# Kernel optimization log

Hardware: AMD Instinct MI355X
Metric: run time of the kernel (lower is better)

Reference implementation:

```python
import jax, jax.numpy as jnp
import numpy as np
from jax import lax

WINDOW_SIZE = 11
SIGMA = 1.5
C1 = 0.01 ** 2
C2 = 0.03 ** 2


def _gaussian_window(channel, window_size, sigma=SIGMA):
    x = jnp.arange(window_size, dtype=jnp.float32)
    g = jnp.exp(-((x - window_size // 2) ** 2) / (2.0 * sigma * sigma))
    g = g / g.sum()
    w2d = jnp.outer(g, g)  # [ws, ws]
    # depthwise kernel in OIHW with feature_group_count=channel: [C, 1, ws, ws]
    return jnp.broadcast_to(w2d[None, None], (channel, 1, window_size, window_size))


def _dwconv(x, window, pad, channel):
    return lax.conv_general_dilated(
        x, window, window_strides=(1, 1), padding=[(pad, pad), (pad, pad)],
        dimension_numbers=("NCHW", "OIHW", "NCHW"), feature_group_count=channel)


def setup_inputs() -> dict:
    key = jax.random.key(0)
    k1, k2 = jax.random.split(key)
    shape = (16, 3, 512, 512)
    img1 = jax.random.uniform(k1, shape, dtype=jnp.float32)
    img2 = jax.random.uniform(k2, shape, dtype=jnp.float32)
    return {"img1": img1, "img2": img2}


def reference(img1, img2):
    _, channel, height, width = img1.shape
    ws = min(WINDOW_SIZE, height, width)
    window = _gaussian_window(channel, ws).astype(img1.dtype)
    pad = WINDOW_SIZE // 2  # matches torch code: padding=window_size // 2

    mu1 = _dwconv(img1, window, pad, channel)
    mu2 = _dwconv(img2, window, pad, channel)
    mu1_sq = mu1 * mu1
    mu2_sq = mu2 * mu2
    mu1_mu2 = mu1 * mu2

    sigma1_sq = _dwconv(img1 * img1, window, pad, channel) - mu1_sq
    sigma2_sq = _dwconv(img2 * img2, window, pad, channel) - mu2_sq
    sigma12 = _dwconv(img1 * img2, window, pad, channel) - mu1_mu2

    ssim_map = ((2.0 * mu1_mu2 + C1) * (2.0 * sigma12 + C2)) / (
        (mu1_sq + mu2_sq + C1) * (sigma1_sq + sigma2_sq + C2))
    return 1.0 - ssim_map.mean()
```

## Files before the change

kernel.cpp:

```cpp
#include <hip/hip_runtime.h>
#include <hip/hip_fp16.h>


#define IMGH 512
#define IMGW 512
#define TW 64
#define TH 32
#define GX 8
#define GY 16
#define GZ 48
#define NBLOCKS (GX * GY * GZ)
#define NPIX (16 * 3 * 512 * 512)
#define C1F 1.0e-4f
#define C2F 9.0e-4f

#define INSTRIDE 88
#define INPLANE (42 * INSTRIDE)
#define VSTRIDE 44
#define VPLANE (64 * VSTRIDE)
#define WBASE 34

#define W0 0.0010283818f
#define W1 0.0075987503f
#define W2 0.0360007547f
#define W3 0.1093606960f
#define W4 0.2130055367f
#define W5 0.2660117184f

typedef _Float16 half8v __attribute__((ext_vector_type(8)));
typedef float f32x4 __attribute__((ext_vector_type(4)));
union H8 { half8v v; __half2 h2[4]; float4 f4; unsigned u[4]; };

static __device__ __forceinline__ __half2 pkrtz(float a, float b) {
    auto r = __builtin_amdgcn_cvt_pkrtz(a, b);
    return *reinterpret_cast<__half2*>(&r);
}
static __device__ __forceinline__ float wval(int i) {
    const float W[11] = {W0, W1, W2, W3, W4, W5, W4, W3, W2, W1, W0};
    float w = 0.f;
#pragma unroll
    for (int j = 0; j < 11; ++j) w = (i == WBASE + j) ? W[j] : w;
    return w;
}

__global__ __launch_bounds__(512, 8)
void ssim_tile(const float* __restrict__ img1, const float* __restrict__ img2,
               float* __restrict__ partials) {
    __shared__ _Float16 sWext[96];
    __shared__ _Float16 sIn[2 * INPLANE];
    __shared__ _Float16 sV[4 * VPLANE];
    __shared__ float wsum[8];

    const int tid  = threadIdx.x;
    const int lane = tid & 63;
    const int wv   = tid >> 6;
    const int lr = lane & 15;
    const int kc = lane >> 4;
    const int r0 = blockIdx.y * TH;
    const int c0 = blockIdx.x * TW;
    const size_t pbase = (size_t)blockIdx.z * (IMGH * IMGW);
    const float* a0 = img1 + pbase;
    const float* b0 = img2 + pbase;
    const bool fast = (blockIdx.x >= 1) & (blockIdx.x <= GX - 2) &
                      (blockIdx.y >= 1) & (blockIdx.y <= GY - 2);

    if (tid < 420) {
        const int row = (unsigned)tid / 10u;
        const int ch  = tid - row * 10;
        const int gr = r0 - 5 + row;
        const int gc = c0 - 8 + 8 * ch;
        f32x4 va1, va2, vb1, vb2;
        if (fast) {
            const float* pa = a0 + (size_t)gr * IMGW + gc;
            const float* pb = b0 + (size_t)gr * IMGW + gc;
            asm volatile(
                "global_load_dwordx4 %0, %4, off\n\t"
                "global_load_dwordx4 %1, %4, off offset:16\n\t"
                "global_load_dwordx4 %2, %5, off\n\t"
                "global_load_dwordx4 %3, %5, off offset:16\n\t"
                "s_waitcnt vmcnt(0)"
                : "=&v"(va1), "=&v"(va2), "=&v"(vb1), "=&v"(vb2)
                : "v"(pa), "v"(pb)
                : "memory");
        } else {
            va1 = (f32x4){0.f, 0.f, 0.f, 0.f};
            va2 = vb1 = vb2 = va1;
            if ((unsigned)gr < IMGH && (unsigned)gc < IMGW) {
                const float* pa = a0 + (size_t)gr * IMGW + gc;
                const float* pb = b0 + (size_t)gr * IMGW + gc;
                va1 = *reinterpret_cast<const f32x4*>(pa);
                va2 = *reinterpret_cast<const f32x4*>(pa + 4);
                vb1 = *reinterpret_cast<const f32x4*>(pb);
                vb2 = *reinterpret_cast<const f32x4*>(pb + 4);
            }
        }
        const int off = row * INSTRIDE + 8 * ch;
        H8 ha, hb;
        ha.h2[0] = pkrtz(va1[0], va1[1]); ha.h2[1] = pkrtz(va1[2], va1[3]);
        ha.h2[2] = pkrtz(va2[0], va2[1]); ha.h2[3] = pkrtz(va2[2], va2[3]);
        hb.h2[0] = pkrtz(vb1[0], vb1[1]); hb.h2[1] = pkrtz(vb1[2], vb1[3]);
        hb.h2[2] = pkrtz(vb2[0], vb2[1]); hb.h2[3] = pkrtz(vb2[2], vb2[3]);
        *reinterpret_cast<float4*>(&sIn[off]) = ha.f4;
        *reinterpret_cast<float4*>(&sIn[INPLANE + off]) = hb.f4;
    } else if (tid >= 448) {
        const int t = tid - 448;
        sWext[t] = (_Float16)wval(t);
        if (t < 32) sWext[t + 64] = (_Float16)wval(t + 64);
#pragma unroll
        for (int j = 0; j < 4; ++j) {
            const int w = t + (j << 6);
            const int q = w >> 6, col = w & 63;
            *reinterpret_cast<unsigned*>(&sV[q * VPLANE + col * VSTRIDE + 42]) = 0u;
        }
    }
    __syncthreads();

    half8v Wh, Av0, Av1;
    {
        const int bi = (kc << 3) - lr + WBASE;
#pragma unroll
        for (int e = 0; e < 8; ++e) Wh[e]  = sWext[bi - 3 + e];
#pragma unroll
        for (int e = 0; e < 8; ++e) Av0[e] = sWext[bi + e];
#pragma unroll
        for (int e = 0; e < 8; ++e) Av1[e] = sWext[bi - 4 + e];
    }

    {
        const int ct = (wv >> 1) & 3;
        const int qp = wv & 1;
#pragma unroll
        for (int rt = 0; rt < 3; ++rt) {
            const int rb = (rt == 0) ? 0 : (rt == 1 ? 16 : 26);
            const int base = (rb + lr) * INSTRIDE + 16 * ct + (kc << 3);
            H8 fa, fb;
            fa.f4 = *reinterpret_cast<const float4*>(&sIn[base]);
            fb.f4 = *reinterpret_cast<const float4*>(&sIn[INPLANE + base]);
            H8 f0, f1;
            if (qp == 0) {
                f0 = fa; f1 = fb;
            } else {
#pragma unroll
                for (int t = 0; t < 4; ++t) {
                    f0.h2[t] = __hfma2(fa.h2[t], fa.h2[t],
                                       __hmul2(fb.h2[t], fb.h2[t]));
                    f1.h2[t] = __hmul2(fa.h2[t], fb.h2[t]);
                }
            }
            f32x4 d0 = {0.f, 0.f, 0.f, 0.f}, d1 = d0;
            d0 = __builtin_amdgcn_mfma_f32_16x16x32_f16(f0.v, Wh, d0, 0, 0, 0);
            d1 = __builtin_amdgcn_mfma_f32_16x16x32_f16(f1.v, Wh, d1, 0, 0, 0);
            const int p0 = qp * 2, p1 = qp * 2 + 1;
            const int vb = (16 * ct + lr) * VSTRIDE + rb + (kc << 2);
            uint2 s0, s1;
            __half2 h;
            h = pkrtz(d0[0], d0[1]); s0.x = *reinterpret_cast<unsigned*>(&h);
            h = pkrtz(d0[2], d0[3]); s0.y = *reinterpret_cast<unsigned*>(&h);
            h = pkrtz(d1[0], d1[1]); s1.x = *reinterpret_cast<unsigned*>(&h);
            h = pkrtz(d1[2], d1[3]); s1.y = *reinterpret_cast<unsigned*>(&h);
            if (rt < 2) {
                *reinterpret_cast<uint2*>(&sV[p0 * VPLANE + vb]) = s0;
                *reinterpret_cast<uint2*>(&sV[p1 * VPLANE + vb]) = s1;
            } else {
                unsigned* q0 = reinterpret_cast<unsigned*>(&sV[p0 * VPLANE + vb]);
                unsigned* q1 = reinterpret_cast<unsigned*>(&sV[p1 * VPLANE + vb]);
                q0[0] = s0.x; q0[1] = s0.y;
                q1[0] = s1.x; q1[1] = s1.y;
            }
        }
    }
    __syncthreads();

    float lsum = 0.f;
    {
        const int ct2 = wv & 3;
        const int rt2 = wv >> 2;
        const int w0 = rt2 ? 12 : 0;
        const half8v Avx = rt2 ? Av1 : Av0;
        const int vbase = (16 * ct2 + lr) * VSTRIDE + w0 + (kc << 3);
        auto vread = [&](int q) -> half8v {
            const _Float16* p = &sV[q * VPLANE + vbase];
            H8 c;
            *reinterpret_cast<uint2*>(&c.u[0]) =
                *reinterpret_cast<const uint2*>(p);
            *reinterpret_cast<uint2*>(&c.u[2]) =
                *reinterpret_cast<const uint2*>(p + 4);
            return c.v;
        };
        f32x4 d0 = {0.f, 0.f, 0.f, 0.f}, d1 = d0, d2 = d0, d3 = d0;
        d0 = __builtin_amdgcn_mfma_f32_16x16x32_f16(Avx, vread(0), d0, 0, 0, 0);
        d1 = __builtin_amdgcn_mfma_f32_16x16x32_f16(Avx, vread(1), d1, 0, 0, 0);
        d2 = __builtin_amdgcn_mfma_f32_16x16x32_f16(Avx, vread(2), d2, 0, 0, 0);
        d3 = __builtin_amdgcn_mfma_f32_16x16x32_f16(Avx, vread(3), d3, 0, 0, 0);
#pragma unroll
        for (int r = 0; r < 4; ++r) {
            const float mu1 = d0[r], mu2 = d1[r], S = d2[r], eab = d3[r];
            const float mu11 = mu1 * mu1, mu22 = mu2 * mu2, mu12 = mu1 * mu2;
            const float s12 = eab - mu12;
            const float num = (2.f * mu12 + C1F) * (2.f * s12 + C2F);
            const float den = (mu11 + mu22 + C1F) * ((S - mu11 - mu22) + C2F);
            lsum += num * __builtin_amdgcn_rcpf(den);
        }
    }

#pragma unroll
    for (int off = 32; off > 0; off >>= 1) lsum += __shfl_down(lsum, off, 64);
    if (lane == 0) wsum[wv] = lsum;
    __syncthreads();
    if (tid == 0) {
        float t = 0.f;
#pragma unroll
        for (int w = 0; w < 8; ++w) t += wsum[w];
        partials[((size_t)blockIdx.z * GY + blockIdx.y) * GX + blockIdx.x] = t;
    }
}

__global__ __launch_bounds__(1024)
void ssim_reduce(const float* __restrict__ partials, float* __restrict__ out, int n) {
    __shared__ float lds[1024];
    float s = 0.f;
    for (int i = threadIdx.x; i < n; i += 1024) s += partials[i];
    lds[threadIdx.x] = s;
    __syncthreads();
    for (int off = 512; off > 0; off >>= 1) {
        if ((int)threadIdx.x < off) lds[threadIdx.x] += lds[threadIdx.x + off];
        __syncthreads();
    }
    if (threadIdx.x == 0) out[0] = 1.f - lds[0] / (float)NPIX;
}

extern "C" void kernel_launch(void* const* d_in, const int* in_sizes, int n_in,
                              void* d_out, int out_size, void* d_ws, size_t ws_size,
                              hipStream_t stream) {
    const float* img1 = (const float*)d_in[0];
    const float* img2 = (const float*)d_in[1];
    float* out = (float*)d_out;
    float* partials = (float*)d_ws;

    dim3 grid(GX, GY, GZ);
    ssim_tile<<<grid, 512, 0, stream>>>(img1, img2, partials);
    ssim_reduce<<<1, 1024, 0, stream>>>(partials, out, NBLOCKS);
}
```

Before: 39.93 us.

## Process four planes per block with register-prefetched global loads

Each block now loops over four image planes instead of one, cutting the grid along z by four. During the compute for the current plane, it issues the global loads for the next plane into registers, so memory latency overlaps the MFMA work. The weight setup is also amortised across the four planes. In exchange there are fewer blocks to fill the GPU, more syncs per block, and the occupancy hint drops from 8 to 6 blocks per CU.

Result: no change. 39.50 us (-1.1%).

```diff
diff --git a/kernel.cpp b/kernel.cpp
--- a/kernel.cpp
+++ b/kernel.cpp
@@ -8,8 +8,8 @@
 #define TH 32
 #define GX 8
 #define GY 16
-#define GZ 48
-#define NBLOCKS (GX * GY * GZ)
+#define GZT 12
+#define NBLOCKS (GX * GY * GZT)
 #define NPIX (16 * 3 * 512 * 512)
 #define C1F 1.0e-4f
 #define C2F 9.0e-4f
@@ -43,7 +43,7 @@
     return w;
 }
 
-__global__ __launch_bounds__(512, 8)
+__global__ __launch_bounds__(512, 6)
 void ssim_tile(const float* __restrict__ img1, const float* __restrict__ img2,
                float* __restrict__ partials) {
     __shared__ _Float16 sWext[96];
@@ -58,148 +58,181 @@
     const int kc = lane >> 4;
     const int r0 = blockIdx.y * TH;
     const int c0 = blockIdx.x * TW;
-    const size_t pbase = (size_t)blockIdx.z * (IMGH * IMGW);
-    const float* a0 = img1 + pbase;
-    const float* b0 = img2 + pbase;
     const bool fast = (blockIdx.x >= 1) & (blockIdx.x <= GX - 2) &
                       (blockIdx.y >= 1) & (blockIdx.y <= GY - 2);
 
-    if (tid < 420) {
-        const int row = (unsigned)tid / 10u;
-        const int ch  = tid - row * 10;
-        const int gr = r0 - 5 + row;
-        const int gc = c0 - 8 + 8 * ch;
-        f32x4 va1, va2, vb1, vb2;
-        if (fast) {
-            const float* pa = a0 + (size_t)gr * IMGW + gc;
-            const float* pb = b0 + (size_t)gr * IMGW + gc;
+    const int prow = (unsigned)tid / 10u;
+    const int pch  = tid - prow * 10;
+    const int pgr  = r0 - 5 + prow;
+    const int pgc  = c0 - 8 + 8 * pch;
+    const bool pok = (unsigned)pgr < IMGH && (unsigned)pgc < IMGW;
+    const size_t goff = (size_t)pgr * IMGW + pgc;
+
+    const float* pa4[4];
+    const float* pb4[4];
+#pragma unroll
+    for (int t = 0; t < 4; ++t) {
+        const size_t pbase = ((size_t)blockIdx.z * 4 + t) * (IMGH * IMGW);
+        pa4[t] = img1 + pbase;
+        pb4[t] = img2 + pbase;
+    }
+
+    if (tid >= 448) {
+        const int t = tid - 448;
+        sWext[t] = (_Float16)wval(t);
+        if (t < 32) sWext[t + 64] = (_Float16)wval(t + 64);
+#pragma unroll
+        for (int j = 0; j < 4; ++j) {
+            const int w = t + (j << 6);
+            const int q = w >> 6, col = w & 63;
+            *reinterpret_cast<unsigned*>(&sV[q * VPLANE + col * VSTRIDE + 42]) = 0u;
+        }
+    }
+
+    f32x4 va1, va2, vb1, vb2;
+    const bool pipeline = fast && (tid < 420);
+
+    if (pipeline) {
+        const float* pa = pa4[0] + goff;
+        const float* pb = pb4[0] + goff;
+        asm volatile(
+            "global_load_dwordx4 %0, %4, off\n\t"
+            "global_load_dwordx4 %1, %4, off offset:16\n\t"
+            "global_load_dwordx4 %2, %5, off\n\t"
+            "global_load_dwordx4 %3, %5, off offset:16"
+            : "=&v"(va1), "=&v"(va2), "=&v"(vb1), "=&v"(vb2)
+            : "v"(pa), "v"(pb)
+            : "memory");
+    }
+
+    half8v Wh, Av0, Av1;
+    float lsum = 0.f;
+
+#pragma unroll
+    for (int t = 0; t < 4; ++t) {
+        if (tid < 420) {
+            if (pipeline) {
+                asm volatile("s_waitcnt vmcnt(0)"
+                             : "+v"(va1), "+v"(va2), "+v"(vb1), "+v"(vb2));
+            } else {
+                va1 = (f32x4){0.f, 0.f, 0.f, 0.f};
+                va2 = vb1 = vb2 = va1;
+                if (pok) {
+                    const float* pa = pa4[t] + goff;
+                    const float* pb = pb4[t] + goff;
+                    va1 = *reinterpret_cast<const f32x4*>(pa);
+                    va2 = *reinterpret_cast<const f32x4*>(pa + 4);
+                    vb1 = *reinterpret_cast<const f32x4*>(pb);
+                    vb2 = *reinterpret_cast<const f32x4*>(pb + 4);
+                }
+            }
+            const int off = prow * INSTRIDE + 8 * pch;
+            H8 ha, hb;
+            ha.h2[0] = pkrtz(va1[0], va1[1]); ha.h2[1] = pkrtz(va1[2], va1[3]);
+            ha.h2[2] = pkrtz(va2[0], va2[1]); ha.h2[3] = pkrtz(va2[2], va2[3]);
+            hb.h2[0] = pkrtz(vb1[0], vb1[1]); hb.h2[1] = pkrtz(vb1[2], vb1[3]);
+            hb.h2[2] = pkrtz(vb2[0], vb2[1]); hb.h2[3] = pkrtz(vb2[2], vb2[3]);
+            *reinterpret_cast<float4*>(&sIn[off]) = ha.f4;
+            *reinterpret_cast<float4*>(&sIn[INPLANE + off]) = hb.f4;
+        }
+        __syncthreads();
+
+        if (t < 3 && pipeline) {
+            const float* pa = pa4[t + 1] + goff;
+            const float* pb = pb4[t + 1] + goff;
             asm volatile(
                 "global_load_dwordx4 %0, %4, off\n\t"
                 "global_load_dwordx4 %1, %4, off offset:16\n\t"
                 "global_load_dwordx4 %2, %5, off\n\t"
-                "global_load_dwordx4 %3, %5, off offset:16\n\t"
-                "s_waitcnt vmcnt(0)"
+                "global_load_dwordx4 %3, %5, off offset:16"
                 : "=&v"(va1), "=&v"(va2), "=&v"(vb1), "=&v"(vb2)
                 : "v"(pa), "v"(pb)
                 : "memory");
-        } else {
-            va1 = (f32x4){0.f, 0.f, 0.f, 0.f};
-            va2 = vb1 = vb2 = va1;
-            if ((unsigned)gr < IMGH && (unsigned)gc < IMGW) {
-                const float* pa = a0 + (size_t)gr * IMGW + gc;
-                const float* pb = b0 + (size_t)gr * IMGW + gc;
-                va1 = *reinterpret_cast<const f32x4*>(pa);
-                va2 = *reinterpret_cast<const f32x4*>(pa + 4);
-                vb1 = *reinterpret_cast<const f32x4*>(pb);
-                vb2 = *reinterpret_cast<const f32x4*>(pb + 4);
-            }
-        }
-        const int off = row * INSTRIDE + 8 * ch;
-        H8 ha, hb;
-        ha.h2[0] = pkrtz(va1[0], va1[1]); ha.h2[1] = pkrtz(va1[2], va1[3]);
-        ha.h2[2] = pkrtz(va2[0], va2[1]); ha.h2[3] = pkrtz(va2[2], va2[3]);
-        hb.h2[0] = pkrtz(vb1[0], vb1[1]); hb.h2[1] = pkrtz(vb1[2], vb1[3]);
-        hb.h2[2] = pkrtz(vb2[0], vb2[1]); hb.h2[3] = pkrtz(vb2[2], vb2[3]);
-        *reinterpret_cast<float4*>(&sIn[off]) = ha.f4;
-        *reinterpret_cast<float4*>(&sIn[INPLANE + off]) = hb.f4;
-    } else if (tid >= 448) {
-        const int t = tid - 448;
-        sWext[t] = (_Float16)wval(t);
-        if (t < 32) sWext[t + 64] = (_Float16)wval(t + 64);
-#pragma unroll
-        for (int j = 0; j < 4; ++j) {
-            const int w = t + (j << 6);
-            const int q = w >> 6, col = w & 63;
-            *reinterpret_cast<unsigned*>(&sV[q * VPLANE + col * VSTRIDE + 42]) = 0u;
-        }
-    }
-    __syncthreads();
-
-    half8v Wh, Av0, Av1;
-    {
-        const int bi = (kc << 3) - lr + WBASE;
-#pragma unroll
-        for (int e = 0; e < 8; ++e) Wh[e]  = sWext[bi - 3 + e];
-#pragma unroll
-        for (int e = 0; e < 8; ++e) Av0[e] = sWext[bi + e];
-#pragma unroll
-        for (int e = 0; e < 8; ++e) Av1[e] = sWext[bi - 4 + e];
-    }
-
-    {
-        const int ct = (wv >> 1) & 3;
-        const int qp = wv & 1;
-#pragma unroll
-        for (int rt = 0; rt < 3; ++rt) {
-            const int rb = (rt == 0) ? 0 : (rt == 1 ? 16 : 26);
-            const int base = (rb + lr) * INSTRIDE + 16 * ct + (kc << 3);
-            H8 fa, fb;
-            fa.f4 = *reinterpret_cast<const float4*>(&sIn[base]);
-            fb.f4 = *reinterpret_cast<const float4*>(&sIn[INPLANE + base]);
-            H8 f0, f1;
-            if (qp == 0) {
-                f0 = fa; f1 = fb;
-            } else {
-#pragma unroll
-                for (int t = 0; t < 4; ++t) {
-                    f0.h2[t] = __hfma2(fa.h2[t], fa.h2[t],
-                                       __hmul2(fb.h2[t], fb.h2[t]));
-                    f1.h2[t] = __hmul2(fa.h2[t], fb.h2[t]);
+        }
+        if (t == 0) {
+            const int bi = (kc << 3) - lr + WBASE;
+#pragma unroll
+            for (int e = 0; e < 8; ++e) Wh[e]  = sWext[bi - 3 + e];
+#pragma unroll
+            for (int e = 0; e < 8; ++e) Av0[e] = sWext[bi + e];
+#pragma unroll
+            for (int e = 0; e < 8; ++e) Av1[e] = sWext[bi - 4 + e];
+        }
+
+        {
+            const int ct = (wv >> 1) & 3;
+            const int qp = wv & 1;
+#pragma unroll
+            for (int rt = 0; rt < 3; ++rt) {
+                const int rb = (rt == 0) ? 0 : (rt == 1 ? 16 : 26);
+                const int base = (rb + lr) * INSTRIDE + 16 * ct + (kc << 3);
+                H8 fa, fb;
+                fa.f4 = *reinterpret_cast<const float4*>(&sIn[base]);
+                fb.f4 = *reinterpret_cast<const float4*>(&sIn[INPLANE + base]);
+                H8 f0, f1;
+                if (qp == 0) {
+                    f0 = fa; f1 = fb;
+                } else {
+#pragma unroll
+                    for (int u = 0; u < 4; ++u) {
+                        f0.h2[u] = __hfma2(fa.h2[u], fa.h2[u],
+                                           __hmul2(fb.h2[u], fb.h2[u]));
+                        f1.h2[u] = __hmul2(fa.h2[u], fb.h2[u]);
+                    }
+                }
+                f32x4 d0 = {0.f, 0.f, 0.f, 0.f}, d1 = d0;
+                d0 = __builtin_amdgcn_mfma_f32_16x16x32_f16(f0.v, Wh, d0, 0, 0, 0);
+                d1 = __builtin_amdgcn_mfma_f32_16x16x32_f16(f1.v, Wh, d1, 0, 0, 0);
+                const int p0 = qp * 2, p1 = qp * 2 + 1;
+                const int vb = (16 * ct + lr) * VSTRIDE + rb + (kc << 2);
+                uint2 s0, s1;
+                __half2 h;
+                h = pkrtz(d0[0], d0[1]); s0.x = *reinterpret_cast<unsigned*>(&h);
+                h = pkrtz(d0[2], d0[3]); s0.y = *reinterpret_cast<unsigned*>(&h);
+                h = pkrtz(d1[0], d1[1]); s1.x = *reinterpret_cast<unsigned*>(&h);
+                h = pkrtz(d1[2], d1[3]); s1.y = *reinterpret_cast<unsigned*>(&h);
+                if (rt < 2) {
+                    *reinterpret_cast<uint2*>(&sV[p0 * VPLANE + vb]) = s0;
+                    *reinterpret_cast<uint2*>(&sV[p1 * VPLANE + vb]) = s1;
+                } else {
+                    unsigned* q0 = reinterpret_cast<unsigned*>(&sV[p0 * VPLANE + vb]);
+                    unsigned* q1 = reinterpret_cast<unsigned*>(&sV[p1 * VPLANE + vb]);
+                    q0[0] = s0.x; q0[1] = s0.y;
+                    q1[0] = s1.x; q1[1] = s1.y;
                 }
             }
-            f32x4 d0 = {0.f, 0.f, 0.f, 0.f}, d1 = d0;
-            d0 = __builtin_amdgcn_mfma_f32_16x16x32_f16(f0.v, Wh, d0, 0, 0, 0);
-            d1 = __builtin_amdgcn_mfma_f32_16x16x32_f16(f1.v, Wh, d1, 0, 0, 0);
-            const int p0 = qp * 2, p1 = qp * 2 + 1;
-            const int vb = (16 * ct + lr) * VSTRIDE + rb + (kc << 2);
-            uint2 s0, s1;
-            __half2 h;
-            h = pkrtz(d0[0], d0[1]); s0.x = *reinterpret_cast<unsigned*>(&h);
-            h = pkrtz(d0[2], d0[3]); s0.y = *reinterpret_cast<unsigned*>(&h);
-            h = pkrtz(d1[0], d1[1]); s1.x = *reinterpret_cast<unsigned*>(&h);
-            h = pkrtz(d1[2], d1[3]); s1.y = *reinterpret_cast<unsigned*>(&h);
-            if (rt < 2) {
-                *reinterpret_cast<uint2*>(&sV[p0 * VPLANE + vb]) = s0;
-                *reinterpret_cast<uint2*>(&sV[p1 * VPLANE + vb]) = s1;
-            } else {
-                unsigned* q0 = reinterpret_cast<unsigned*>(&sV[p0 * VPLANE + vb]);
-                unsigned* q1 = reinterpret_cast<unsigned*>(&sV[p1 * VPLANE + vb]);
-                q0[0] = s0.x; q0[1] = s0.y;
-                q1[0] = s1.x; q1[1] = s1.y;
+        }
+        __syncthreads();
+
+        {
+            const int ct2 = wv & 3;
+            const int rt2 = wv >> 2;
+            const int w0 = rt2 ? 12 : 0;
+            const half8v Avx = rt2 ? Av1 : Av0;
+            const int vbase = (16 * ct2 + lr) * VSTRIDE + w0 + (kc << 3);
+            auto vread = [&](int q) -> half8v {
+                const _Float16* p = &sV[q * VPLANE + vbase];
+                H8 c;
+                *reinterpret_cast<uint2*>(&c.u[0]) =
+                    *reinterpret_cast<const uint2*>(p);
+                *reinterpret_cast<uint2*>(&c.u[2]) =
+                    *reinterpret_cast<const uint2*>(p + 4);
+                return c.v;
+            };
+            f32x4 d0 = {0.f, 0.f, 0.f, 0.f}, d1 = d0, d2 = d0, d3 = d0;
+            d0 = __builtin_amdgcn_mfma_f32_16x16x32_f16(Avx, vread(0), d0, 0, 0, 0);
+            d1 = __builtin_amdgcn_mfma_f32_16x16x32_f16(Avx, vread(1), d1, 0, 0, 0);
+            d2 = __builtin_amdgcn_mfma_f32_16x16x32_f16(Avx, vread(2), d2, 0, 0, 0);
+            d3 = __builtin_amdgcn_mfma_f32_16x16x32_f16(Avx, vread(3), d3, 0, 0, 0);
+#pragma unroll
+            for (int r = 0; r < 4; ++r) {
+                const float mu1 = d0[r], mu2 = d1[r], S = d2[r], eab = d3[r];
+                const float mu11 = mu1 * mu1, mu22 = mu2 * mu2, mu12 = mu1 * mu2;
+                const float s12 = eab - mu12;
+                const float num = (2.f * mu12 + C1F) * (2.f * s12 + C2F);
+                const float den = (mu11 + mu22 + C1F) * ((S - mu11 - mu22) + C2F);
+                lsum += num * __builtin_amdgcn_rcpf(den);
             }
-        }
-    }
-    __syncthreads();
-
-    float lsum = 0.f;
-    {
-        const int ct2 = wv & 3;
-        const int rt2 = wv >> 2;
-        const int w0 = rt2 ? 12 : 0;
-        const half8v Avx = rt2 ? Av1 : Av0;
-        const int vbase = (16 * ct2 + lr) * VSTRIDE + w0 + (kc << 3);
-        auto vread = [&](int q) -> half8v {
-            const _Float16* p = &sV[q * VPLANE + vbase];
-            H8 c;
-            *reinterpret_cast<uint2*>(&c.u[0]) =
-                *reinterpret_cast<const uint2*>(p);
-            *reinterpret_cast<uint2*>(&c.u[2]) =
-                *reinterpret_cast<const uint2*>(p + 4);
-            return c.v;
-        };
-        f32x4 d0 = {0.f, 0.f, 0.f, 0.f}, d1 = d0, d2 = d0, d3 = d0;
-        d0 = __builtin_amdgcn_mfma_f32_16x16x32_f16(Avx, vread(0), d0, 0, 0, 0);
-        d1 = __builtin_amdgcn_mfma_f32_16x16x32_f16(Avx, vread(1), d1, 0, 0, 0);
-        d2 = __builtin_amdgcn_mfma_f32_16x16x32_f16(Avx, vread(2), d2, 0, 0, 0);
-        d3 = __builtin_amdgcn_mfma_f32_16x16x32_f16(Avx, vread(3), d3, 0, 0, 0);
-#pragma unroll
-        for (int r = 0; r < 4; ++r) {
-            const float mu1 = d0[r], mu2 = d1[r], S = d2[r], eab = d3[r];
-            const float mu11 = mu1 * mu1, mu22 = mu2 * mu2, mu12 = mu1 * mu2;
-            const float s12 = eab - mu12;
-            const float num = (2.f * mu12 + C1F) * (2.f * s12 + C2F);
-            const float den = (mu11 + mu22 + C1F) * ((S - mu11 - mu22) + C2F);
-            lsum += num * __builtin_amdgcn_rcpf(den);
         }
     }
 
@@ -237,7 +270,7 @@
     float* out = (float*)d_out;
     float* partials = (float*)d_ws;
 
-    dim3 grid(GX, GY, GZ);
+    dim3 grid(GX, GY, GZT);
     ssim_tile<<<grid, 512, 0, stream>>>(img1, img2, partials);
     ssim_reduce<<<1, 1024, 0, stream>>>(partials, out, NBLOCKS);
 }
```
